# Optimization experiments

Measured on AMD Instinct MI355X. Metric: run time of the kernel, lower is better.

Reference implementation:

```python
import jax, jax.numpy as jnp
import numpy as np

B, T, I, H = 4, 512, 128, 128


def _lstm(x, Wih, Whh, b):
    """Standard LSTM (PyTorch gate order i,f,g,o). x: [B,T,I] -> h: [B,T,H]."""
    xg = jnp.swapaxes(x, 0, 1) @ Wih.T + b  # [T,B,4H] input projections precomputed
    Hh = Whh.shape[1]
    h0 = jnp.zeros((x.shape[0], Hh), x.dtype)
    c0 = jnp.zeros((x.shape[0], Hh), x.dtype)

    def step(carry, xg_t):
        h, c = carry
        g = xg_t + h @ Whh.T
        i, f, gg, o = jnp.split(g, 4, axis=-1)
        c = jax.nn.sigmoid(f) * c + jax.nn.sigmoid(i) * jnp.tanh(gg)
        h = jax.nn.sigmoid(o) * jnp.tanh(c)
        return (h, c), h

    _, hs = jax.lax.scan(step, (h0, c0), xg)
    return jnp.swapaxes(hs, 0, 1)  # [B,T,H]


def setup_inputs() -> dict:
    key = jax.random.key(0)
    ks = jax.random.split(key, 12)
    s = 0.1
    return {
        "x": jax.random.normal(ks[0], (B, T, I), jnp.float32),
        # shared LSTM
        "Wih_s": jax.random.normal(ks[1], (4 * H, I), jnp.float32) * s,
        "Whh_s": jax.random.normal(ks[2], (4 * H, H), jnp.float32) * s,
        "b_lstm_s": jnp.zeros((4 * H,), jnp.float32),
        # Ws split along its concatenated input [x_sub; h_t; h_sub]
        "Wx": jax.random.normal(ks[3], (I, H), jnp.float32) * s,
        "Wht": jax.random.normal(ks[4], (H, H), jnp.float32) * s,
        "Whs": jax.random.normal(ks[5], (H, H), jnp.float32) * s,
        "bs": jnp.zeros((H,), jnp.float32),
        # Us: H -> 1
        "u": jax.random.normal(ks[6], (H,), jnp.float32) * s,
        "bu": jnp.zeros((), jnp.float32),
        # task LSTM over [x; R] (input_size + hidden_size)
        "Wih_t": jax.random.normal(ks[7], (4 * H, I + H), jnp.float32) * s,
        "Whh_t": jax.random.normal(ks[8], (4 * H, H), jnp.float32) * s,
        "b_lstm_t": jnp.zeros((4 * H,), jnp.float32),
    }


def reference(x, Wih_s, Whh_s, b_lstm_s, Wx, Wht, Whs, bs, u, bu,
              Wih_t, Whh_t, b_lstm_t):
    # 1) shared LSTM encoding
    Hsh = _lstm(x, Wih_s, Whh_s, b_lstm_s)  # [B,T,H]

    # 2) pairwise attention scores S[b,t,s] = Us(tanh(Ws([x_s; h_t; h_s])))
    #    decompose Ws over its concatenated input to avoid building the concat
    xp = x @ Wx          # [B,T,H] (indexed by s)
    hp_t = Hsh @ Wht     # [B,T,H] (indexed by t)
    hp_s = Hsh @ Whs     # [B,T,H] (indexed by s)
    # M[b,t,s,:]: [B,T,T,H] — the dominant (memory-bound) intermediate
    M = jnp.tanh(hp_t[:, :, None, :] + (xp + hp_s)[:, None, :, :] + bs)
    scores = jnp.einsum("btsh,h->bts", M, u) + bu  # [B,T,T]

    # 3) softmax over sub_t and weighted sum of shared outputs
    beta = jax.nn.softmax(scores, axis=-1)         # [B,T,T]
    R = jnp.einsum("bts,bsh->bth", beta, Hsh)      # [B,T,H]

    # 4) task-specific LSTM consuming the input and the aggregated message
    h_task = _lstm(jnp.concatenate([x, R], axis=-1), Wih_t, Whh_t, b_lstm_t)
    return h_task  # [B,T,H]
```

## Files before the change

### kernel.cpp

```cpp
#include <hip/hip_runtime.h>
#include <hip/hip_bf16.h>
#include <math.h>

#define Bq 4
#define Tq 512
#define Hq 128

typedef _Float16 f16x4 __attribute__((ext_vector_type(4)));
typedef _Float16 f16x8 __attribute__((ext_vector_type(8)));
typedef float f32x4 __attribute__((ext_vector_type(4)));

__device__ __forceinline__ float rcp_fast(float x) { return __builtin_amdgcn_rcpf(x); }
__device__ __forceinline__ float sigmoid_fast(float x) {
    return rcp_fast(1.0f + __expf(-x));
}
__device__ __forceinline__ float tanh_fast(float x) {
    float e = __expf(2.0f * x);
    return 1.0f - 2.0f * rcp_fast(e + 1.0f);
}

__device__ __forceinline__ void gemm_nt_body(float (*As)[68], float (*Ws)[68],
                                             const float* __restrict__ A, int lda,
                                             const float* __restrict__ W, int ldw,
                                             const float* __restrict__ bias,
                                             float* __restrict__ C, int acc_flag,
                                             int m0, int n0, int tid) {
    int tx = tid & 15, ty = tid >> 4;
    float acc[4][4] = {};
    for (int kc = 0; kc < 2; kc++) {
        __syncthreads();
#pragma unroll
        for (int i = 0; i < 4; i++) {
            int idx = tid + 256 * i;
            int r = idx >> 4, c4 = idx & 15;
            *(float4*)(&As[r][c4 * 4]) = *(const float4*)(A + (size_t)(m0 + r) * lda + kc * 64 + c4 * 4);
            *(float4*)(&Ws[r][c4 * 4]) = *(const float4*)(W + (size_t)(n0 + r) * ldw + kc * 64 + c4 * 4);
        }
        __syncthreads();
#pragma unroll
        for (int k4 = 0; k4 < 16; k4++) {
            float4 a[4], wv[4];
#pragma unroll
            for (int i = 0; i < 4; i++) a[i] = *(const float4*)(&As[ty * 4 + i][k4 * 4]);
#pragma unroll
            for (int j = 0; j < 4; j++) wv[j] = *(const float4*)(&Ws[tx * 4 + j][k4 * 4]);
#pragma unroll
            for (int i = 0; i < 4; i++)
#pragma unroll
                for (int j = 0; j < 4; j++)
                    acc[i][j] += a[i].x * wv[j].x + a[i].y * wv[j].y + a[i].z * wv[j].z + a[i].w * wv[j].w;
        }
    }
#pragma unroll
    for (int i = 0; i < 4; i++) {
        int m = m0 + ty * 4 + i;
        int n = n0 + tx * 4;
        float4 v = make_float4(acc[i][0], acc[i][1], acc[i][2], acc[i][3]);
        if (bias) { v.x += bias[n]; v.y += bias[n + 1]; v.z += bias[n + 2]; v.w += bias[n + 3]; }
        if (acc_flag) {
            float4 o = *(const float4*)(C + (size_t)m * 512 + n);
            v.x += o.x; v.y += o.y; v.z += o.z; v.w += o.w;
        }
        *(float4*)(C + (size_t)m * 512 + n) = v;
    }
}

__device__ __forceinline__ void gemm_nt_512(float (*As)[68], float (*Ws)[68],
                                            const float* __restrict__ A, int lda,
                                            const float* __restrict__ W, int ldw,
                                            const float* __restrict__ bias,
                                            float* __restrict__ C,
                                            int m0, int n0, int tid) {
    int tx = tid & 15, ty = tid >> 4;
    float acc[2][4] = {};
    for (int kc = 0; kc < 2; kc++) {
        __syncthreads();
#pragma unroll
        for (int i = 0; i < 2; i++) {
            int idx = tid + 512 * i;
            int r = idx >> 4, c4 = idx & 15;
            *(float4*)(&As[r][c4 * 4]) = *(const float4*)(A + (size_t)(m0 + r) * lda + kc * 64 + c4 * 4);
            *(float4*)(&Ws[r][c4 * 4]) = *(const float4*)(W + (size_t)(n0 + r) * ldw + kc * 64 + c4 * 4);
        }
        __syncthreads();
#pragma unroll
        for (int k4 = 0; k4 < 16; k4++) {
            float4 a[2], wv[4];
#pragma unroll
            for (int i = 0; i < 2; i++) a[i] = *(const float4*)(&As[ty * 2 + i][k4 * 4]);
#pragma unroll
            for (int j = 0; j < 4; j++) wv[j] = *(const float4*)(&Ws[tx * 4 + j][k4 * 4]);
#pragma unroll
            for (int i = 0; i < 2; i++)
#pragma unroll
                for (int j = 0; j < 4; j++)
                    acc[i][j] += a[i].x * wv[j].x + a[i].y * wv[j].y + a[i].z * wv[j].z + a[i].w * wv[j].w;
        }
    }
#pragma unroll
    for (int i = 0; i < 2; i++) {
        int m = m0 + ty * 2 + i;
        int n = n0 + tx * 4;
        float4 v = make_float4(acc[i][0], acc[i][1], acc[i][2], acc[i][3]);
        if (bias) { v.x += bias[n]; v.y += bias[n + 1]; v.z += bias[n + 2]; v.w += bias[n + 3]; }
        *(float4*)(C + (size_t)m * 512 + n) = v;
    }
}

__global__ __launch_bounds__(256) void prep(const float* __restrict__ x,
                                            const float* __restrict__ Wih_s,
                                            const float* __restrict__ b_s,
                                            const float* __restrict__ Whh_s,
                                            float* __restrict__ xg_s,
                                            _Float16* __restrict__ W16_s) {
    __shared__ __align__(16) float As[64][68];
    __shared__ __align__(16) float Ws[64][68];
    int bid = blockIdx.x;
    int tid = threadIdx.x;
    if (bid < 256) {
        gemm_nt_body(As, Ws, x, 128, Wih_s, 128, b_s, xg_s, 0,
                     (bid & 31) * 64, (bid >> 5) * 64, tid);
    } else {
        int cb = bid - 256;
        int i = (cb * 256 + tid) * 4;
        float4 v = *(const float4*)(Whh_s + i);
        f16x4 o;
        o[0] = (_Float16)v.x; o[1] = (_Float16)v.y;
        o[2] = (_Float16)v.z; o[3] = (_Float16)v.w;
        *(f16x4*)(W16_s + i) = o;
    }
}

__global__ __launch_bounds__(256) void gemm_nt(const float* __restrict__ A, int lda,
                                               const float* __restrict__ W, int ldw,
                                               const float* __restrict__ bias,
                                               float* __restrict__ C, int acc_flag) {
    __shared__ __align__(16) float As[64][68];
    __shared__ __align__(16) float Ws[64][68];
    gemm_nt_body(As, Ws, A, lda, W, ldw, bias, C, acc_flag,
                 blockIdx.x * 64, blockIdx.y * 64, threadIdx.x);
}

__global__ __launch_bounds__(256) void mid(const float* __restrict__ x,
                                           const float* __restrict__ Hsh,
                                           const float* __restrict__ Wht,
                                           const float* __restrict__ Wx,
                                           const float* __restrict__ Whs,
                                           const float* __restrict__ bs,
                                           float* __restrict__ hp_t,
                                           float* __restrict__ c_s) {
    __shared__ __align__(16) float As[64][68];
    __shared__ __align__(16) float Bs[64][68];
    int bid = blockIdx.x;
    int cfg = bid >> 6;
    int b2 = bid & 63;
    int m0 = (b2 & 31) * 64, n0 = (b2 >> 5) * 64;
    const float* A1 = cfg ? x : Hsh;
    const float* B1 = cfg ? Wx : Wht;
    const float* A2 = cfg ? Hsh : nullptr;
    const float* B2 = cfg ? Whs : nullptr;
    const float* bias = cfg ? bs : nullptr;
    float* C = cfg ? c_s : hp_t;

    int tid = threadIdx.x;
    int tx = tid & 15, ty = tid >> 4;
    float acc[4][4] = {};
    for (int src = 0; src < 2; src++) {
        const float* A = src ? A2 : A1;
        const float* Bm = src ? B2 : B1;
        if (!A) break;
        for (int kc = 0; kc < 2; kc++) {
            __syncthreads();
#pragma unroll
            for (int i = 0; i < 4; i++) {
                int idx = tid + 256 * i;
                int r = idx >> 4, c4 = idx & 15;
                *(float4*)(&As[r][c4 * 4]) = *(const float4*)(A + (size_t)(m0 + r) * 128 + kc * 64 + c4 * 4);
                *(float4*)(&Bs[r][c4 * 4]) = *(const float4*)(Bm + (size_t)(kc * 64 + r) * 128 + n0 + c4 * 4);
            }
            __syncthreads();
#pragma unroll
            for (int k4 = 0; k4 < 16; k4++) {
                float4 a[4];
#pragma unroll
                for (int i = 0; i < 4; i++) a[i] = *(const float4*)(&As[ty * 4 + i][k4 * 4]);
#pragma unroll
                for (int kk = 0; kk < 4; kk++) {
                    float4 bv = *(const float4*)(&Bs[k4 * 4 + kk][tx * 4]);
#pragma unroll
                    for (int i = 0; i < 4; i++) {
                        float av = (kk == 0) ? a[i].x : (kk == 1) ? a[i].y : (kk == 2) ? a[i].z : a[i].w;
                        acc[i][0] += av * bv.x;
                        acc[i][1] += av * bv.y;
                        acc[i][2] += av * bv.z;
                        acc[i][3] += av * bv.w;
                    }
                }
            }
        }
    }
#pragma unroll
    for (int i = 0; i < 4; i++) {
        int m = m0 + ty * 4 + i;
        int n = n0 + tx * 4;
        float4 v = make_float4(acc[i][0], acc[i][1], acc[i][2], acc[i][3]);
        if (bias) { v.x += bias[n]; v.y += bias[n + 1]; v.z += bias[n + 2]; v.w += bias[n + 3]; }
        *(float4*)(C + (size_t)m * 128 + n) = v;
    }
}

#define MF0(ACC, A, B) \
    asm("v_mfma_f32_16x16x32_f16 %0, %1, %2, %3" : "=&v"(ACC) : "v"(A), "a"(B), "v"(zro));
#define MF(ACC, A, B) \
    asm("v_mfma_f32_16x16x32_f16 %0, %1, %2, %0" : "+v"(ACC) : "v"(A), "a"(B));

#define LSTM_STEP(X0, X1, X2, X3, R0, R1, R2, R3, WPTR, PXG)                       \
    {                                                                              \
        f16x8 a0 = *(R0); f16x8 a1 = *(R1);                                        \
        f16x8 a2 = *(R2); f16x8 a3 = *(R3);                                        \
        float o0 = X0, o1 = X1, o2 = X2, o3 = X3;                                  \
        X0 = (PXG)[0]; X1 = (PXG)[128]; X2 = (PXG)[256]; X3 = (PXG)[384];          \
        (PXG) += 1024;                                                             \
        f32x4 ac0a, ac1a, ac2a, ac3a, ac0b, ac1b, ac2b, ac3b;                      \
        MF0(ac0a, a0, b00) MF0(ac1a, a0, b10) MF0(ac2a, a0, b20) MF0(ac3a, a0, b30)\
        MF0(ac0b, a2, b02) MF0(ac1b, a2, b12) MF0(ac2b, a2, b22) MF0(ac3b, a2, b32)\
        MF(ac0a, a1, b01) MF(ac1a, a1, b11) MF(ac2a, a1, b21) MF(ac3a, a1, b31)    \
        MF(ac0b, a3, b03) MF(ac1b, a3, b13) MF(ac2b, a3, b23) MF(ac3b, a3, b33)    \
            \
        __builtin_amdgcn_sched_barrier(0);                                         \
        asm volatile("s_nop 7\n\ts_nop 7"                                          \
                     :: "v"(ac0a), "v"(ac1a), "v"(ac2a), "v"(ac3a),                \
                        "v"(ac0b), "v"(ac1b), "v"(ac2b), "v"(ac3b));               \
        __builtin_amdgcn_sched_barrier(0);                                         \
        float gi = ac0a[0] + ac0b[0] + o0;                                         \
        float gf = ac1a[0] + ac1b[0] + o1;                                         \
        float gg = ac2a[0] + ac2b[0] + o2;                                         \
        float go = ac3a[0] + ac3b[0] + o3;                                         \
        float si = sigmoid_fast(gi), sf = sigmoid_fast(gf), so = sigmoid_fast(go); \
        float tg = tanh_fast(gg);                                                  \
        c = sf * c + si * tg;                                                      \
        float h = so * tanh_fast(c);                                               \
        *(WPTR) = (_Float16)h;                                                     \
        *pH = h; pH += Hq;                                                         \
        __builtin_amdgcn_sched_barrier(0);                                         \
        asm volatile("s_waitcnt lgkmcnt(0)");                                      \
        __builtin_amdgcn_s_barrier();                                              \
        __builtin_amdgcn_sched_barrier(0);                                         \
    }

__device__ __forceinline__ void lstm_core(const float* __restrict__ xg,
                                          const _Float16* __restrict__ W16,
                                          float* __restrict__ Hout,
                                          _Float16* hbase, int tid) {
    int w = tid >> 6, lane = tid & 63;
    int r = lane & 15, kg = lane >> 4;
    int ch = 16 * w + r;

    for (int i = tid; i < 4096; i += 512) hbase[i] = (_Float16)0.f;

    const _Float16* wb = W16 + (size_t)ch * 128 + kg * 8;
#define LWB(g, kb) *(const f16x8*)(wb + (size_t)(g) * 16384 + (kb) * 32)
    f16x8 b00 = LWB(0, 0), b01 = LWB(0, 1), b02 = LWB(0, 2), b03 = LWB(0, 3);
    f16x8 b10 = LWB(1, 0), b11 = LWB(1, 1), b12 = LWB(1, 2), b13 = LWB(1, 3);
    f16x8 b20 = LWB(2, 0), b21 = LWB(2, 1), b22 = LWB(2, 2), b23 = LWB(2, 3);
    f16x8 b30 = LWB(3, 0), b31 = LWB(3, 1), b32 = LWB(3, 2), b33 = LWB(3, 3);
#undef LWB
    f32x4 zro = {0.f, 0.f, 0.f, 0.f};
    asm volatile(""
                 : "+a"(b00), "+a"(b01), "+a"(b02), "+a"(b03),
                   "+a"(b10), "+a"(b11), "+a"(b12), "+a"(b13),
                   "+a"(b20), "+a"(b21), "+a"(b22), "+a"(b23),
                   "+a"(b30), "+a"(b31), "+a"(b32), "+a"(b33),
                   "+v"(zro));

    int aoff0 = r * 128 + (((0 * 4 + kg) ^ r) << 3);
    int aoff1 = r * 128 + (((1 * 4 + kg) ^ r) << 3);
    int aoff2 = r * 128 + (((2 * 4 + kg) ^ r) << 3);
    int aoff3 = r * 128 + (((3 * 4 + kg) ^ r) << 3);
    int woff = (4 * kg) * 128 + (((ch >> 3) ^ (4 * kg)) << 3) + (ch & 7);

    const f16x8* rA0 = (const f16x8*)(hbase + aoff0);
    const f16x8* rA1 = (const f16x8*)(hbase + aoff1);
    const f16x8* rA2 = (const f16x8*)(hbase + aoff2);
    const f16x8* rA3 = (const f16x8*)(hbase + aoff3);
    const f16x8* rB0 = (const f16x8*)(hbase + 2048 + aoff0);
    const f16x8* rB1 = (const f16x8*)(hbase + 2048 + aoff1);
    const f16x8* rB2 = (const f16x8*)(hbase + 2048 + aoff2);
    const f16x8* rB3 = (const f16x8*)(hbase + 2048 + aoff3);
    _Float16* wA = hbase + 2048 + woff;
    _Float16* wB = hbase + woff;

    size_t kgTq = (size_t)kg * Tq;
    const float* p0 = xg + (kgTq + 0) * 512 + ch;
    const float* p1 = xg + (kgTq + 1) * 512 + ch;
    float xa0 = p0[0], xa1 = p0[128], xa2 = p0[256], xa3 = p0[384];
    float xb0 = p1[0], xb1 = p1[128], xb2 = p1[256], xb3 = p1[384];
    const float* pA = xg + (kgTq + 2) * 512 + ch;
    const float* pB = xg + (kgTq + 3) * 512 + ch;
    float* pH = Hout + kgTq * Hq + ch;

    float c = 0.f;
    __syncthreads();

    for (int t = 0; t < Tq; t += 2) {
        LSTM_STEP(xa0, xa1, xa2, xa3, rA0, rA1, rA2, rA3, wA, pA)
        LSTM_STEP(xb0, xb1, xb2, xb3, rB0, rB1, rB2, rB3, wB, pB)
    }
}

__global__ __launch_bounds__(512)
__attribute__((amdgpu_waves_per_eu(2, 2)))
void lstm_fused(const float* __restrict__ xg_s,
                const _Float16* __restrict__ W16_s,
                float* __restrict__ Hsh,
                const float* __restrict__ x,
                const float* __restrict__ Wih_t,
                const float* __restrict__ b_t,
                const float* __restrict__ Whh_t,
                float* __restrict__ xg_t,
                _Float16* __restrict__ W16_t) {
    __shared__ __align__(16) float smem[2][64][68];
    int bid = blockIdx.x;
    int tid = threadIdx.x;
    if (bid == 0) {
        lstm_core(xg_s, W16_s, Hsh, (_Float16*)&smem[0][0][0], tid);
    } else if (bid <= 256) {
        int b2 = bid - 1;
        gemm_nt_512(smem[0], smem[1], x, 128, Wih_t, 256, b_t, xg_t,
                    (b2 & 31) * 64, (b2 >> 5) * 64, tid);
    } else {
        int cb = bid - 257;
        int i = (cb * 512 + tid) * 2;
        float2 v = *(const float2*)(Whh_t + i);
        W16_t[i] = (_Float16)v.x;
        W16_t[i + 1] = (_Float16)v.y;
    }
}

__global__ __launch_bounds__(512)
__attribute__((amdgpu_waves_per_eu(2, 2)))
void lstm_b4(const float* __restrict__ xg,
             const _Float16* __restrict__ W16,
             float* __restrict__ Hout) {
    __shared__ _Float16 hbuf[2][16][128];
    lstm_core(xg, W16, Hout, &hbuf[0][0][0], threadIdx.x);
}

__global__ __launch_bounds__(256) void attn_kernel(const float* __restrict__ hp_t,
                                                   const float* __restrict__ c_s,
                                                   const float* __restrict__ u,
                                                   const float* __restrict__ Hsh,
                                                   float* __restrict__ R) {
    int t = blockIdx.x, b = blockIdx.y;
    int tid = threadIdx.x;
    __shared__ __align__(16) float a_lds[128];
    __shared__ __align__(16) float u_lds[128];
    __shared__ __align__(16) float sc[512];
    __shared__ __align__(16) float red[256];

    if (tid < 128) {
        a_lds[tid] = hp_t[((size_t)b * Tq + t) * Hq + tid];
        u_lds[tid] = u[tid];
    }
    __syncthreads();

    int lane = tid & 63, wv = tid >> 6;
    int h4 = lane & 15, s2 = lane >> 4;
    float4 a0 = *(const float4*)(&a_lds[h4 * 4]);
    float4 a1 = *(const float4*)(&a_lds[64 + h4 * 4]);
    float4 u0 = *(const float4*)(&u_lds[h4 * 4]);
    float4 u1 = *(const float4*)(&u_lds[64 + h4 * 4]);

    const float* cb = c_s + (size_t)b * Tq * Hq;
    float psum = 0.0f;
#pragma unroll 4
    for (int it = 0; it < 32; ++it) {
        int s = it * 16 + wv * 4 + s2;
        const float4* crow = (const float4*)(cb + (size_t)s * Hq);
        float4 c0 = crow[h4];
        float4 c1 = crow[h4 + 16];
        float acc = u0.x * tanh_fast(a0.x + c0.x) + u0.y * tanh_fast(a0.y + c0.y)
                  + u0.z * tanh_fast(a0.z + c0.z) + u0.w * tanh_fast(a0.w + c0.w)
                  + u1.x * tanh_fast(a1.x + c1.x) + u1.y * tanh_fast(a1.y + c1.y)
                  + u1.z * tanh_fast(a1.z + c1.z) + u1.w * tanh_fast(a1.w + c1.w);
        acc += __shfl_xor(acc, 1, 64);
        acc += __shfl_xor(acc, 2, 64);
        acc += __shfl_xor(acc, 4, 64);
        acc += __shfl_xor(acc, 8, 64);
        if (h4 == 0) {
            float p = __expf(acc);
            sc[s] = p;
            psum += p;
        }
    }
#pragma unroll
    for (int off = 1; off < 64; off <<= 1) psum += __shfl_xor(psum, off, 64);
    if (lane == 0) red[wv] = psum;
    __syncthreads();
    float rinv = rcp_fast(red[0] + red[1] + red[2] + red[3]);

    int h = tid & 127, half = tid >> 7;
    float acc = 0.0f;
    for (int s = half; s < 512; s += 2) {
        acc += sc[s] * Hsh[((size_t)b * Tq + s) * Hq + h];
    }
    red[tid] = acc;
    __syncthreads();
    if (tid < 128) {
        R[((size_t)b * Tq + t) * Hq + tid] = (red[tid] + red[tid + 128]) * rinv;
    }
}

extern "C" void kernel_launch(void* const* d_in, const int* in_sizes, int n_in,
                              void* d_out, int out_size, void* d_ws, size_t ws_size,
                              hipStream_t stream) {
    const float* x      = (const float*)d_in[0];
    const float* Wih_s  = (const float*)d_in[1];
    const float* Whh_s  = (const float*)d_in[2];
    const float* b_s    = (const float*)d_in[3];
    const float* Wx     = (const float*)d_in[4];
    const float* Wht    = (const float*)d_in[5];
    const float* Whs    = (const float*)d_in[6];
    const float* bs     = (const float*)d_in[7];
    const float* u      = (const float*)d_in[8];
    const float* Wih_t  = (const float*)d_in[10];
    const float* Whh_t  = (const float*)d_in[11];
    const float* b_t    = (const float*)d_in[12];
    float* out = (float*)d_out;

    float* ws    = (float*)d_ws;
    float* xg_s  = ws;
    float* xg_t  = ws + 1048576;
    float* Hsh   = ws + 2097152;
    float* hp_t  = ws + 2359296;
    float* c_s   = ws + 2621440;
    float* Rbuf  = ws + 2883584;
    _Float16* W16_t = (_Float16*)(ws + 3145728);
    _Float16* W16_s = (_Float16*)hp_t;

    dim3 blk(256);

    prep<<<320, blk, 0, stream>>>(x, Wih_s, b_s, Whh_s, xg_s, W16_s);

    lstm_fused<<<321, 512, 0, stream>>>(xg_s, W16_s, Hsh,
                                        x, Wih_t, b_t, Whh_t, xg_t, W16_t);

    mid<<<128, blk, 0, stream>>>(x, Hsh, Wht, Wx, Whs, bs, hp_t, c_s);

    attn_kernel<<<dim3(Tq, Bq), blk, 0, stream>>>(hp_t, c_s, u, Hsh, Rbuf);

    gemm_nt<<<dim3(32, 8), blk, 0, stream>>>(Rbuf, 128, Wih_t + 128, 256, nullptr, xg_t, 1);

    lstm_b4<<<1, 512, 0, stream>>>(xg_t, W16_t, out);
}
```

Baseline: 623.7 us.

## Store c_s transposed and compute attention scores per-thread without shuffles

The mid kernel now writes the s-indexed projection in a transposed [B,H,T] layout through LDS. The attention kernel assigns one key position s per thread (two per thread) and loops over h, so loads are coalesced across s and the per-row shuffle reduction disappears. tanh is folded algebraically: u·tanh(a+c) becomes a constant term plus -2u/(exp(2(a+c))+1), with 2a and -2u precomputed in LDS. The dropped constant sum(u) cancels under the softmax. The cost is an LDS transpose in mid and a serial 128-step loop per thread.

Result: no change. 615.5 us (-1.3%).

```diff
diff --git a/kernel.cpp b/kernel.cpp
--- a/kernel.cpp
+++ b/kernel.cpp
@@ -148,7 +148,7 @@
                                            const float* __restrict__ Whs,
                                            const float* __restrict__ bs,
                                            float* __restrict__ hp_t,
-                                           float* __restrict__ c_s) {
+                                           float* __restrict__ c_sT) {
     __shared__ __align__(16) float As[64][68];
     __shared__ __align__(16) float Bs[64][68];
     int bid = blockIdx.x;
@@ -159,8 +159,6 @@
     const float* B1 = cfg ? Wx : Wht;
     const float* A2 = cfg ? Hsh : nullptr;
     const float* B2 = cfg ? Whs : nullptr;
-    const float* bias = cfg ? bs : nullptr;
-    float* C = cfg ? c_s : hp_t;
 
     int tid = threadIdx.x;
     int tx = tid & 15, ty = tid >> 4;
@@ -199,13 +197,30 @@
             }
         }
     }
-#pragma unroll
-    for (int i = 0; i < 4; i++) {
-        int m = m0 + ty * 4 + i;
-        int n = n0 + tx * 4;
-        float4 v = make_float4(acc[i][0], acc[i][1], acc[i][2], acc[i][3]);
-        if (bias) { v.x += bias[n]; v.y += bias[n + 1]; v.z += bias[n + 2]; v.w += bias[n + 3]; }
-        *(float4*)(C + (size_t)m * 128 + n) = v;
+    if (cfg == 0) {
+#pragma unroll
+        for (int i = 0; i < 4; i++) {
+            int m = m0 + ty * 4 + i;
+            int n = n0 + tx * 4;
+            *(float4*)(hp_t + (size_t)m * 128 + n) =
+                make_float4(acc[i][0], acc[i][1], acc[i][2], acc[i][3]);
+        }
+    } else {
+        __syncthreads();
+#pragma unroll
+        for (int i = 0; i < 4; i++)
+#pragma unroll
+            for (int j = 0; j < 4; j++)
+                As[ty * 4 + i][tx * 4 + j] = acc[i][j] + bs[n0 + tx * 4 + j];
+        __syncthreads();
+        int b = m0 >> 9;
+        int s0 = m0 & 511;
+        int lane = tid & 63, wv = tid >> 6;
+#pragma unroll 4
+        for (int it = 0; it < 16; ++it) {
+            int nl = wv * 16 + it;
+            c_sT[((size_t)(b * 128 + n0 + nl)) * 512 + s0 + lane] = As[lane][nl];
+        }
     }
 }
 
@@ -226,7 +241,6 @@
         MF0(ac0b, a2, b02) MF0(ac1b, a2, b12) MF0(ac2b, a2, b22) MF0(ac3b, a2, b32)\
         MF(ac0a, a1, b01) MF(ac1a, a1, b11) MF(ac2a, a1, b21) MF(ac3a, a1, b31)    \
         MF(ac0b, a3, b03) MF(ac1b, a3, b13) MF(ac2b, a3, b23) MF(ac3b, a3, b33)    \
-            \
         __builtin_amdgcn_sched_barrier(0);                                         \
         asm volatile("s_nop 7\n\ts_nop 7"                                          \
                      :: "v"(ac0a), "v"(ac1a), "v"(ac2a), "v"(ac3a),                \
@@ -347,54 +361,44 @@
 }
 
 __global__ __launch_bounds__(256) void attn_kernel(const float* __restrict__ hp_t,
-                                                   const float* __restrict__ c_s,
+                                                   const float* __restrict__ c_sT,
                                                    const float* __restrict__ u,
                                                    const float* __restrict__ Hsh,
                                                    float* __restrict__ R) {
     int t = blockIdx.x, b = blockIdx.y;
     int tid = threadIdx.x;
-    __shared__ __align__(16) float a_lds[128];
-    __shared__ __align__(16) float u_lds[128];
+    __shared__ __align__(16) float a2_lds[128];
+    __shared__ __align__(16) float un2_lds[128];
     __shared__ __align__(16) float sc[512];
     __shared__ __align__(16) float red[256];
 
     if (tid < 128) {
-        a_lds[tid] = hp_t[((size_t)b * Tq + t) * Hq + tid];
-        u_lds[tid] = u[tid];
+        a2_lds[tid] = 2.0f * hp_t[((size_t)b * Tq + t) * Hq + tid];
+        un2_lds[tid] = -2.0f * u[tid];
     }
     __syncthreads();
 
+    const float* pc = c_sT + (size_t)b * 65536 + tid;
+    float acc0 = 0.f, acc1 = 0.f;
+#pragma unroll 4
+    for (int h = 0; h < 128; ++h) {
+        float c0 = pc[0];
+        float c1 = pc[256];
+        float a2 = a2_lds[h], un2 = un2_lds[h];
+        float e0 = __expf(fmaf(2.0f, c0, a2));
+        float e1 = __expf(fmaf(2.0f, c1, a2));
+        acc0 = fmaf(un2, rcp_fast(e0 + 1.0f), acc0);
+        acc1 = fmaf(un2, rcp_fast(e1 + 1.0f), acc1);
+        pc += 512;
+    }
+    float p0 = __expf(acc0), p1 = __expf(acc1);
+    sc[tid] = p0;
+    sc[tid + 256] = p1;
+
+    float psum = p0 + p1;
+#pragma unroll
+    for (int off = 1; off < 64; off <<= 1) psum += __shfl_xor(psum, off, 64);
     int lane = tid & 63, wv = tid >> 6;
-    int h4 = lane & 15, s2 = lane >> 4;
-    float4 a0 = *(const float4*)(&a_lds[h4 * 4]);
-    float4 a1 = *(const float4*)(&a_lds[64 + h4 * 4]);
-    float4 u0 = *(const float4*)(&u_lds[h4 * 4]);
-    float4 u1 = *(const float4*)(&u_lds[64 + h4 * 4]);
-
-    const float* cb = c_s + (size_t)b * Tq * Hq;
-    float psum = 0.0f;
-#pragma unroll 4
-    for (int it = 0; it < 32; ++it) {
-        int s = it * 16 + wv * 4 + s2;
-        const float4* crow = (const float4*)(cb + (size_t)s * Hq);
-        float4 c0 = crow[h4];
-        float4 c1 = crow[h4 + 16];
-        float acc = u0.x * tanh_fast(a0.x + c0.x) + u0.y * tanh_fast(a0.y + c0.y)
-                  + u0.z * tanh_fast(a0.z + c0.z) + u0.w * tanh_fast(a0.w + c0.w)
-                  + u1.x * tanh_fast(a1.x + c1.x) + u1.y * tanh_fast(a1.y + c1.y)
-                  + u1.z * tanh_fast(a1.z + c1.z) + u1.w * tanh_fast(a1.w + c1.w);
-        acc += __shfl_xor(acc, 1, 64);
-        acc += __shfl_xor(acc, 2, 64);
-        acc += __shfl_xor(acc, 4, 64);
-        acc += __shfl_xor(acc, 8, 64);
-        if (h4 == 0) {
-            float p = __expf(acc);
-            sc[s] = p;
-            psum += p;
-        }
-    }
-#pragma unroll
-    for (int off = 1; off < 64; off <<= 1) psum += __shfl_xor(psum, off, 64);
     if (lane == 0) red[wv] = psum;
     __syncthreads();
     float rinv = rcp_fast(red[0] + red[1] + red[2] + red[3]);
@@ -433,7 +437,7 @@
     float* xg_t  = ws + 1048576;
     float* Hsh   = ws + 2097152;
     float* hp_t  = ws + 2359296;
-    float* c_s   = ws + 2621440;
+    float* c_sT  = ws + 2621440;
     float* Rbuf  = ws + 2883584;
     _Float16* W16_t = (_Float16*)(ws + 3145728);
     _Float16* W16_s = (_Float16*)hp_t;
@@ -445,9 +449,9 @@
     lstm_fused<<<321, 512, 0, stream>>>(xg_s, W16_s, Hsh,
                                         x, Wih_t, b_t, Whh_t, xg_t, W16_t);
 
-    mid<<<128, blk, 0, stream>>>(x, Hsh, Wht, Wx, Whs, bs, hp_t, c_s);
-
-    attn_kernel<<<dim3(Tq, Bq), blk, 0, stream>>>(hp_t, c_s, u, Hsh, Rbuf);
+    mid<<<128, blk, 0, stream>>>(x, Hsh, Wht, Wx, Whs, bs, hp_t, c_sT);
+
+    attn_kernel<<<dim3(Tq, Bq), blk, 0, stream>>>(hp_t, c_sT, u, Hsh, Rbuf);
 
     gemm_nt<<<dim3(32, 8), blk, 0, stream>>>(Rbuf, 128, Wih_t + 128, 256, nullptr, xg_t, 1);
 
```
